# Kernel optimization log

Measured on AMD Instinct MI355X. Metric: run time of the kernel, lower is better.

The kernel has to match this reference:

```python
import jax, jax.numpy as jnp
import numpy as np

EPS = 1e-3  # keras LayerNormalization default epsilon
D_INNER = 64


def setup_inputs() -> dict:
    key = jax.random.key(0)
    ks = jax.random.split(key, 5)
    B, N, M, C = 4, 1024, 32, 128
    x = jax.random.normal(ks[0], (B, N, M, C), dtype=jnp.float32)
    # Glorot-uniform init bounds
    lim_qk = float(np.sqrt(6.0 / (C + D_INNER)))
    lim_v = float(np.sqrt(6.0 / (C + C)))
    w_q = jax.random.uniform(ks[1], (C, D_INNER), jnp.float32, -lim_qk, lim_qk)
    w_k = jax.random.uniform(ks[2], (C, D_INNER), jnp.float32, -lim_qk, lim_qk)
    w_v = jax.random.uniform(ks[3], (C, C), jnp.float32, -lim_v, lim_v)
    lam = jnp.full((C,), 0.1, dtype=jnp.float32)  # lam_init_eps default eps=0.1
    gamma = jnp.ones((C,), dtype=jnp.float32)
    beta = jnp.zeros((C,), dtype=jnp.float32)
    return {"x": x, "gamma": gamma, "beta": beta, "w_q": w_q, "w_k": w_k,
            "w_v": w_v, "lam": lam}


def reference(x, gamma, beta, w_q, w_k, w_v, lam):
    # LayerNorm over channel axis C
    mean = jnp.mean(x, axis=-1, keepdims=True)
    var = jnp.mean(jnp.square(x - mean), axis=-1, keepdims=True)
    xn = (x - mean) * jax.lax.rsqrt(var + EPS) * gamma + beta  # [B,N,M,C]
    xn = jnp.transpose(xn, (0, 2, 1, 3))  # [B,M,N,C] attention over N per feature
    q = jnp.einsum('bmnc,cd->bmnd', xn, w_q)
    k = jnp.einsum('bmnc,cd->bmnd', xn, w_k)
    scores = jnp.einsum('bmnd,bmkd->bmnk', q, k) / jnp.sqrt(
        jnp.asarray(D_INNER, dtype=jnp.float32))
    A = jax.nn.softmax(scores, axis=-1)  # [B,M,N,N]
    v = jnp.einsum('bmnc,ce->bmne', xn, w_v)  # [B,M,N,C]
    attn = jnp.einsum('bmnk,bmkc->bmnc', A, v)
    attn = jnp.transpose(attn, (0, 2, 1, 3))  # back to [B,N,M,C]
    return x + attn * lam
```

## Files before the change

### kernel.cpp

```cpp
#include <hip/hip_runtime.h>
#include <hip/hip_bf16.h>

#define B_ 4
#define N_ 1024
#define M_ 32
#define C_ 128
#define D_ 64
#define BM_ (B_*M_)

typedef float f32x4 __attribute__((ext_vector_type(4)));
typedef float f32x16 __attribute__((ext_vector_type(16)));
typedef short short8 __attribute__((ext_vector_type(8)));
typedef short short4v __attribute__((ext_vector_type(4)));

#define EXP2(x) __builtin_amdgcn_exp2f(x)

static __device__ __forceinline__ int cvtpk_bf16(float lo, float hi) {
  int r;
  asm volatile("v_cvt_pk_bf16_f32 %0, %1, %2" : "=v"(r) : "v"(lo), "v"(hi));
  return r;
}
static __device__ __forceinline__ void plswap(int& a, int& b) {
  asm volatile("v_permlane32_swap_b32 %0, %1" : "+v"(a), "+v"(b));
}

__global__ __launch_bounds__(256) void prep_weights(
    const float* __restrict__ wq, const float* __restrict__ wk,
    const float* __restrict__ wv, __hip_bfloat16* __restrict__ wt) {
  int idx = blockIdx.x * 256 + threadIdx.x;
  int col = idx >> 7;
  int kk  = idx & 127;
  float v;
  if (col < 64)        v = wq[kk * 64 + col] * (0.125f * 1.44269504088896f);
  else if (col < 128)  v = wk[kk * 64 + (col - 64)];
  else                 v = wv[kk * 128 + (col - 128)];
  wt[col * 128 + kk] = __float2bfloat16(v);
}

__global__ __launch_bounds__(512, 6) void ln_qkv(
    const float* __restrict__ x, const float* __restrict__ gamma,
    const float* __restrict__ beta, const __hip_bfloat16* __restrict__ wt,
    __hip_bfloat16* __restrict__ q, __hip_bfloat16* __restrict__ k,
    __hip_bfloat16* __restrict__ vt) {
  __shared__ alignas(16) __hip_bfloat16 xn[128][136];

  int bid = blockIdx.x;
  int bm  = bid >> 3;
  int n0  = (bid & 7) * 128;
  int b   = bm >> 5, m = bm & 31;
  int tid = threadIdx.x;

  const float* xbase = x + ((((size_t)b * N_ + n0) * M_ + m) * C_);
  int c4 = tid & 31;
  float4 vch[8];
  #pragma unroll
  for (int it = 0; it < 8; ++it) {
    int r = (it * 512 + tid) >> 5;
    vch[it] = *reinterpret_cast<const float4*>(xbase + (size_t)r * (M_ * C_) + c4 * 4);
  }
  float4 g4 = *reinterpret_cast<const float4*>(gamma + c4 * 4);
  float4 b4 = *reinterpret_cast<const float4*>(beta + c4 * 4);

  #pragma unroll
  for (int it = 0; it < 8; ++it) {
    int r = (it * 512 + tid) >> 5;
    float4 v = vch[it];
    float s  = (v.x + v.y) + (v.z + v.w);
    float sq = (v.x * v.x + v.y * v.y) + (v.z * v.z + v.w * v.w);
    s  += __shfl_xor(s, 1);  sq += __shfl_xor(sq, 1);
    s  += __shfl_xor(s, 2);  sq += __shfl_xor(sq, 2);
    s  += __shfl_xor(s, 4);  sq += __shfl_xor(sq, 4);
    s  += __shfl_xor(s, 8);  sq += __shfl_xor(sq, 8);
    s  += __shfl_xor(s, 16); sq += __shfl_xor(sq, 16);
    float mean = s * (1.f / 128.f);
    float var  = sq * (1.f / 128.f) - mean * mean;
    float rstd = rsqrtf(var + 1e-3f);
    alignas(8) __hip_bfloat16 tmp[4];
    tmp[0] = __float2bfloat16((v.x - mean) * rstd * g4.x + b4.x);
    tmp[1] = __float2bfloat16((v.y - mean) * rstd * g4.y + b4.y);
    tmp[2] = __float2bfloat16((v.z - mean) * rstd * g4.z + b4.z);
    tmp[3] = __float2bfloat16((v.w - mean) * rstd * g4.w + b4.w);
    *reinterpret_cast<short4v*>(&xn[r][c4 * 4]) =
        *reinterpret_cast<const short4v*>(tmp);
  }
  __syncthreads();

  int w = tid >> 6, l = tid & 63, lr = l & 15, lh = l >> 4;
  int ct0 = w, ct1 = w + 8;

  short8 wf0[4], wf1[4];
  #pragma unroll
  for (int h = 0; h < 4; ++h) {
    wf0[h] = *reinterpret_cast<const short8*>(
        &wt[(ct0 * 16 + lr) * 128 + h * 32 + lh * 8]);
    wf1[h] = *reinterpret_cast<const short8*>(
        &wt[(ct1 * 16 + lr) * 128 + h * 32 + lh * 8]);
  }

  const f32x4 fzero = {0.f, 0.f, 0.f, 0.f};
  int col0 = ct0 * 16 + lr;
  int cV   = w * 16 + lr;
  #pragma unroll
  for (int rt = 0; rt < 8; ++rt) {
    short8 a[4];
    #pragma unroll
    for (int h = 0; h < 4; ++h)
      a[h] = *reinterpret_cast<const short8*>(&xn[rt * 16 + lr][h * 32 + lh * 8]);
    f32x4 acc0 = fzero, acc1 = fzero;
    #pragma unroll
    for (int h = 0; h < 4; ++h) {
      acc0 = __builtin_amdgcn_mfma_f32_16x16x32_bf16(a[h], wf0[h], acc0, 0, 0, 0);
      acc1 = __builtin_amdgcn_mfma_f32_16x16x32_bf16(a[h], wf1[h], acc1, 0, 0, 0);
    }
    int nb = n0 + rt * 16 + lh * 4;
    if (ct0 < 4) {
      #pragma unroll
      for (int r = 0; r < 4; ++r)
        q[((size_t)bm * N_ + nb + r) * D_ + col0] = __float2bfloat16(acc0[r]);
    } else {
      #pragma unroll
      for (int r = 0; r < 4; ++r)
        k[((size_t)bm * N_ + nb + r) * D_ + (col0 - 64)] = __float2bfloat16(acc0[r]);
    }
    alignas(8) __hip_bfloat16 tmp[4];
    #pragma unroll
    for (int r = 0; r < 4; ++r) tmp[r] = __float2bfloat16(acc1[r]);
    *reinterpret_cast<short4v*>(&vt[((size_t)bm * C_ + cV) * N_ + nb]) =
        *reinterpret_cast<const short4v*>(tmp);
  }
}

__global__ __launch_bounds__(256, 2) void attn_kernel(
    const float* __restrict__ x, const float* __restrict__ lam,
    const __hip_bfloat16* __restrict__ q, const __hip_bfloat16* __restrict__ k,
    const __hip_bfloat16* __restrict__ vt, float* __restrict__ out) {
  __shared__ alignas(16) __hip_bfloat16 vbuf[2][128 * 72];

  int h   = blockIdx.x;
  int s_  = h >> 3;
  int bm  = (s_ >> 3) * 8 + (h & 7);
  int n0  = (s_ & 7) * 128;
  int b   = bm >> 5, m = bm & 31;
  int tid = threadIdx.x;
  int w = tid >> 6, l = tid & 63;
  int lq = l & 31, hi = l >> 5;

  const __hip_bfloat16* kbase = k + (size_t)bm * N_ * D_;
  const __hip_bfloat16* vbase = vt + (size_t)bm * C_ * N_;

  const __hip_bfloat16* kp0 = kbase + (size_t)lq * D_ + hi * 8;
  const __hip_bfloat16* kp1 = kbase + (size_t)(32 + lq) * D_ + hi * 8;

  int vr[4], vc = tid & 7;
  #pragma unroll
  for (int i = 0; i < 4; ++i) vr[i] = (tid + i * 256) >> 3;

  short8 qf[4];
  {
    int n = n0 + w * 32 + lq;
    const __hip_bfloat16* qp = q + ((size_t)bm * N_ + n) * D_;
    #pragma unroll
    for (int s = 0; s < 4; ++s)
      qf[s] = *reinterpret_cast<const short8*>(qp + s * 16 + hi * 8);
  }

  f32x16 acc[4];
  const f32x16 z16 = {0.f,0.f,0.f,0.f,0.f,0.f,0.f,0.f,
                      0.f,0.f,0.f,0.f,0.f,0.f,0.f,0.f};
  #pragma unroll
  for (int ct = 0; ct < 4; ++ct) acc[ct] = z16;
  float m_run = -1e30f, l_run = 0.f;

  short8 vreg[4];
  #pragma unroll
  for (int i = 0; i < 4; ++i)
    vreg[i] = *reinterpret_cast<const short8*>(&vbase[(size_t)vr[i] * N_ + vc * 8]);
  #pragma unroll
  for (int i = 0; i < 4; ++i)
    *reinterpret_cast<short8*>(&vbuf[0][vr[i] * 72 + vc * 8]) = vreg[i];
  __syncthreads();

  for (int t = 0; t < 16; ++t) {
    int cur = t & 1, nxt = cur ^ 1;
    int j0 = t * 64;

    short8 kf0[4], kf1[4];
    #pragma unroll
    for (int s = 0; s < 4; ++s) {
      kf0[s] = *reinterpret_cast<const short8*>(kp0 + (size_t)j0 * D_ + s * 16);
      kf1[s] = *reinterpret_cast<const short8*>(kp1 + (size_t)j0 * D_ + s * 16);
    }
    if (t < 15) {
      int j0n = j0 + 64;
      #pragma unroll
      for (int i = 0; i < 4; ++i)
        vreg[i] = *reinterpret_cast<const short8*>(&vbase[(size_t)vr[i] * N_ + j0n + vc * 8]);
    }

    const __hip_bfloat16* vtt = vbuf[cur];

    f32x16 st[2];
    st[0] = z16; st[1] = z16;
    #pragma unroll
    for (int s = 0; s < 4; ++s) {
      st[0] = __builtin_amdgcn_mfma_f32_32x32x16_bf16(kf0[s], qf[s], st[0], 0, 0, 0);
      st[1] = __builtin_amdgcn_mfma_f32_32x32x16_bf16(kf1[s], qf[s], st[1], 0, 0, 0);
    }

    float mx;
    {
      float t8[8];
      #pragma unroll
      for (int i = 0; i < 8; ++i)
        t8[i] = fmaxf(fmaxf(st[0][i], st[0][i + 8]), fmaxf(st[1][i], st[1][i + 8]));
      float a0 = fmaxf(fmaxf(t8[0], t8[1]), fmaxf(t8[2], t8[3]));
      float a1 = fmaxf(fmaxf(t8[4], t8[5]), fmaxf(t8[6], t8[7]));
      mx = fmaxf(a0, a1);
      mx = fmaxf(mx, __shfl_xor(mx, 32));
    }
    if (__any(mx > m_run + 8.0f)) {
      float mnew = fmaxf(m_run, mx);
      float fac = EXP2(m_run - mnew);
      l_run *= fac;
      m_run = mnew;
      #pragma unroll
      for (int reg = 0; reg < 16; ++reg) {
        int qi = (reg & 3) + 8 * (reg >> 2) + 4 * hi;
        float f = __shfl(fac, qi);
        #pragma unroll
        for (int ct = 0; ct < 4; ++ct) acc[ct][reg] *= f;
      }
    }
    #pragma unroll
    for (int i = 0; i < 16; ++i) {
      st[0][i] = EXP2(st[0][i] - m_run);
      st[1][i] = EXP2(st[1][i] - m_run);
    }
    {
      float s8[8];
      #pragma unroll
      for (int i = 0; i < 8; ++i)
        s8[i] = (st[0][i] + st[0][i + 8]) + (st[1][i] + st[1][i + 8]);
      float rs = ((s8[0] + s8[1]) + (s8[2] + s8[3])) +
                 ((s8[4] + s8[5]) + (s8[6] + s8[7]));
      rs += __shfl_xor(rs, 32);
      l_run += rs;
    }

    union W4 { int w[4]; short8 s8; } pf[4];
    #pragma unroll
    for (int t32 = 0; t32 < 2; ++t32) {
      int A = cvtpk_bf16(st[t32][0], st[t32][1]);
      int Bw = cvtpk_bf16(st[t32][2], st[t32][3]);
      int Cw = cvtpk_bf16(st[t32][4], st[t32][5]);
      int Dw = cvtpk_bf16(st[t32][6], st[t32][7]);
      plswap(A, Cw);
      plswap(Bw, Dw);
      pf[t32 * 2].w[0] = A;  pf[t32 * 2].w[1] = Bw;
      pf[t32 * 2].w[2] = Cw; pf[t32 * 2].w[3] = Dw;
      int E = cvtpk_bf16(st[t32][8], st[t32][9]);
      int F = cvtpk_bf16(st[t32][10], st[t32][11]);
      int G = cvtpk_bf16(st[t32][12], st[t32][13]);
      int H = cvtpk_bf16(st[t32][14], st[t32][15]);
      plswap(E, G);
      plswap(F, H);
      pf[t32 * 2 + 1].w[0] = E; pf[t32 * 2 + 1].w[1] = F;
      pf[t32 * 2 + 1].w[2] = G; pf[t32 * 2 + 1].w[3] = H;
    }

    #pragma unroll
    for (int kb = 0; kb < 4; ++kb) {
      #pragma unroll
      for (int ct = 0; ct < 4; ++ct) {
        short8 vf = *reinterpret_cast<const short8*>(
            &vtt[(ct * 32 + lq) * 72 + kb * 16 + hi * 8]);
        acc[ct] = __builtin_amdgcn_mfma_f32_32x32x16_bf16(pf[kb].s8, vf, acc[ct], 0, 0, 0);
      }
    }

    if (t < 15) {
      #pragma unroll
      for (int i = 0; i < 4; ++i)
        *reinterpret_cast<short8*>(&vbuf[nxt][vr[i] * 72 + vc * 8]) = vreg[i];
      __syncthreads();
    }
  }

  float inv = 1.0f / l_run;
  float rlv[16];
  #pragma unroll
  for (int reg = 0; reg < 16; ++reg) {
    int qi = (reg & 3) + 8 * (reg >> 2) + 4 * hi;
    rlv[reg] = __shfl(inv, qi);
  }
  #pragma unroll
  for (int ct = 0; ct < 4; ++ct) {
    int c = ct * 32 + lq;
    float lamc = lam[c];
    #pragma unroll
    for (int reg = 0; reg < 16; ++reg) {
      int qi = (reg & 3) + 8 * (reg >> 2) + 4 * hi;
      int n = n0 + w * 32 + qi;
      size_t idx = ((((size_t)b * N_ + n) * M_ + m) * C_) + c;
      out[idx] = x[idx] + acc[ct][reg] * rlv[reg] * lamc;
    }
  }
}

extern "C" void kernel_launch(void* const* d_in, const int* in_sizes, int n_in,
                              void* d_out, int out_size, void* d_ws, size_t ws_size,
                              hipStream_t stream) {
  const float* x     = (const float*)d_in[0];
  const float* gamma = (const float*)d_in[1];
  const float* beta  = (const float*)d_in[2];
  const float* wq    = (const float*)d_in[3];
  const float* wk    = (const float*)d_in[4];
  const float* wv    = (const float*)d_in[5];
  const float* lam   = (const float*)d_in[6];
  float* out = (float*)d_out;

  __hip_bfloat16* ws = (__hip_bfloat16*)d_ws;
  __hip_bfloat16* wt = ws;
  __hip_bfloat16* q  = wt + 256 * 128;
  __hip_bfloat16* k  = q + (size_t)BM_ * N_ * D_;
  __hip_bfloat16* vt = k + (size_t)BM_ * N_ * D_;

  prep_weights<<<128, 256, 0, stream>>>(wq, wk, wv, wt);
  ln_qkv<<<BM_ * (N_ / 128), 512, 0, stream>>>(x, gamma, beta, wt, q, k, vt);
  attn_kernel<<<BM_ * (N_ / 128), 256, 0, stream>>>(x, lam, q, k, vt, out);
}
```

Baseline: 131.7 us.

## Stage K tiles through double-buffered LDS and single-buffer V tile

Each 64-row K tile is now loaded cooperatively by the whole block into a double-buffered LDS array. Warps then read their K fragments from LDS instead of each warp loading the same K rows from global memory, which removes the redundant per-warp global K traffic. To keep the LDS footprint the same, V drops to a single buffer. That adds an extra block barrier per iteration before V is overwritten, so there are more synchronisation points in the main loop.

After: 112.4 us. 1.17x faster.

```diff
diff --git a/kernel.cpp b/kernel.cpp
--- a/kernel.cpp
+++ b/kernel.cpp
@@ -134,7 +134,8 @@
     const float* __restrict__ x, const float* __restrict__ lam,
     const __hip_bfloat16* __restrict__ q, const __hip_bfloat16* __restrict__ k,
     const __hip_bfloat16* __restrict__ vt, float* __restrict__ out) {
-  __shared__ alignas(16) __hip_bfloat16 vbuf[2][128 * 72];
+  __shared__ alignas(16) __hip_bfloat16 kbuf[2][64 * 72];
+  __shared__ alignas(16) __hip_bfloat16 vbuf[128 * 72];
 
   int h   = blockIdx.x;
   int s_  = h >> 3;
@@ -148,9 +149,8 @@
   const __hip_bfloat16* kbase = k + (size_t)bm * N_ * D_;
   const __hip_bfloat16* vbase = vt + (size_t)bm * C_ * N_;
 
-  const __hip_bfloat16* kp0 = kbase + (size_t)lq * D_ + hi * 8;
-  const __hip_bfloat16* kp1 = kbase + (size_t)(32 + lq) * D_ + hi * 8;
-
+  int kr0 = tid >> 3,          kc = tid & 7;
+  int kr1 = (tid + 256) >> 3;
   int vr[4], vc = tid & 7;
   #pragma unroll
   for (int i = 0; i < 4; ++i) vr[i] = (tid + i * 256) >> 3;
@@ -171,40 +171,40 @@
   for (int ct = 0; ct < 4; ++ct) acc[ct] = z16;
   float m_run = -1e30f, l_run = 0.f;
 
-  short8 vreg[4];
+  short8 kreg[2], vreg[4];
+  kreg[0] = *reinterpret_cast<const short8*>(&kbase[(size_t)kr0 * D_ + kc * 8]);
+  kreg[1] = *reinterpret_cast<const short8*>(&kbase[(size_t)kr1 * D_ + kc * 8]);
   #pragma unroll
   for (int i = 0; i < 4; ++i)
     vreg[i] = *reinterpret_cast<const short8*>(&vbase[(size_t)vr[i] * N_ + vc * 8]);
+  *reinterpret_cast<short8*>(&kbuf[0][kr0 * 72 + kc * 8]) = kreg[0];
+  *reinterpret_cast<short8*>(&kbuf[0][kr1 * 72 + kc * 8]) = kreg[1];
   #pragma unroll
   for (int i = 0; i < 4; ++i)
-    *reinterpret_cast<short8*>(&vbuf[0][vr[i] * 72 + vc * 8]) = vreg[i];
+    *reinterpret_cast<short8*>(&vbuf[vr[i] * 72 + vc * 8]) = vreg[i];
   __syncthreads();
 
   for (int t = 0; t < 16; ++t) {
     int cur = t & 1, nxt = cur ^ 1;
-    int j0 = t * 64;
-
-    short8 kf0[4], kf1[4];
-    #pragma unroll
-    for (int s = 0; s < 4; ++s) {
-      kf0[s] = *reinterpret_cast<const short8*>(kp0 + (size_t)j0 * D_ + s * 16);
-      kf1[s] = *reinterpret_cast<const short8*>(kp1 + (size_t)j0 * D_ + s * 16);
-    }
     if (t < 15) {
-      int j0n = j0 + 64;
+      int j0n = (t + 1) * 64;
+      kreg[0] = *reinterpret_cast<const short8*>(&kbase[(size_t)(j0n + kr0) * D_ + kc * 8]);
+      kreg[1] = *reinterpret_cast<const short8*>(&kbase[(size_t)(j0n + kr1) * D_ + kc * 8]);
       #pragma unroll
       for (int i = 0; i < 4; ++i)
         vreg[i] = *reinterpret_cast<const short8*>(&vbase[(size_t)vr[i] * N_ + j0n + vc * 8]);
     }
 
-    const __hip_bfloat16* vtt = vbuf[cur];
+    const __hip_bfloat16* kt = kbuf[cur];
 
     f32x16 st[2];
     st[0] = z16; st[1] = z16;
     #pragma unroll
     for (int s = 0; s < 4; ++s) {
-      st[0] = __builtin_amdgcn_mfma_f32_32x32x16_bf16(kf0[s], qf[s], st[0], 0, 0, 0);
-      st[1] = __builtin_amdgcn_mfma_f32_32x32x16_bf16(kf1[s], qf[s], st[1], 0, 0, 0);
+      short8 kf0 = *reinterpret_cast<const short8*>(&kt[lq * 72 + s * 16 + hi * 8]);
+      st[0] = __builtin_amdgcn_mfma_f32_32x32x16_bf16(kf0, qf[s], st[0], 0, 0, 0);
+      short8 kf1 = *reinterpret_cast<const short8*>(&kt[(32 + lq) * 72 + s * 16 + hi * 8]);
+      st[1] = __builtin_amdgcn_mfma_f32_32x32x16_bf16(kf1, qf[s], st[1], 0, 0, 0);
     }
 
     float mx;
@@ -268,21 +268,28 @@
       pf[t32 * 2 + 1].w[2] = G; pf[t32 * 2 + 1].w[3] = H;
     }
 
+    if (t < 15) {
+      *reinterpret_cast<short8*>(&kbuf[nxt][kr0 * 72 + kc * 8]) = kreg[0];
+      *reinterpret_cast<short8*>(&kbuf[nxt][kr1 * 72 + kc * 8]) = kreg[1];
+    }
+
+    __syncthreads();
+
     #pragma unroll
     for (int kb = 0; kb < 4; ++kb) {
       #pragma unroll
       for (int ct = 0; ct < 4; ++ct) {
         short8 vf = *reinterpret_cast<const short8*>(
-            &vtt[(ct * 32 + lq) * 72 + kb * 16 + hi * 8]);
+            &vbuf[(ct * 32 + lq) * 72 + kb * 16 + hi * 8]);
         acc[ct] = __builtin_amdgcn_mfma_f32_32x32x16_bf16(pf[kb].s8, vf, acc[ct], 0, 0, 0);
       }
     }
 
     if (t < 15) {
+      __syncthreads();
       #pragma unroll
       for (int i = 0; i < 4; ++i)
-        *reinterpret_cast<short8*>(&vbuf[nxt][vr[i] * 72 + vc * 8]) = vreg[i];
-      __syncthreads();
+        *reinterpret_cast<short8*>(&vbuf[vr[i] * 72 + vc * 8]) = vreg[i];
     }
   }
 
```
